# Performance work log

Hardware: AMD Instinct MI355X
Metric: run time of the kernel (lower is better)

The kernel has to match this reference:

```python
import jax, jax.numpy as jnp
import numpy as np

R = 16
ALPHA = 32.0
SCALING = ALPHA / R


def setup_inputs() -> dict:
    key = jax.random.key(0)
    ks = jax.random.split(key, 6)
    B, T, C, O, E = 16, 1500, 1024, 1024, 8
    x = jax.random.normal(ks[0], (B, T, C), dtype=jnp.float32)
    # gate weights per batch element (e.g. softmax-like, but module accepts any)
    w = jax.random.uniform(ks[1], (B, E), dtype=jnp.float32)
    W_base = jax.random.normal(ks[2], (O, C), dtype=jnp.float32) * 0.02
    b_base = jax.random.normal(ks[3], (O,), dtype=jnp.float32) * 0.02
    As = jax.random.normal(ks[4], (E, R, C), dtype=jnp.float32) * 0.02
    Bs = jax.random.normal(ks[5], (E, O, R), dtype=jnp.float32) * 0.02
    return {"x": x, "w": w, "W_base": W_base, "b_base": b_base, "As": As, "Bs": Bs}


def reference(x, w, W_base, b_base, As, Bs):
    # base linear: (B,T,C) @ (C,O) + b
    out = jnp.einsum('btc,oc->bto', x, W_base) + b_base
    # per-expert low-rank: h[b,t,e,r] = x[b,t,:] @ A_e^T
    h = jnp.einsum('btc,erc->bter', x, As)          # (B,T,E,R)
    # y[b,t,e,o] = h @ B_e^T ; gate-weighted sum over experts
    lora = jnp.einsum('bter,eor,be->bto', h, Bs, w)  # (B,T,O)
    return out + lora * SCALING
```

## Files before the change

### kernel.cpp

```cpp
#include <hip/hip_runtime.h>
#include <stdint.h>
#include <stddef.h>


#define B_ 16
#define T_ 1500
#define C_ 1024
#define O_ 1024
#define E_ 8
#define R_ 16
#define ER 128
#define KK 1152
#define BT 24000
#define SCALING 2.0f

typedef __bf16 bf16x8 __attribute__((ext_vector_type(8)));
typedef float f32x4 __attribute__((ext_vector_type(4)));
typedef unsigned short u16;

__device__ inline u16 f2bf(float f) {
  union { float f; unsigned u; } v; v.f = f;
  unsigned u = v.u;
  u += 0x7fff + ((u >> 16) & 1);
  return (u16)(u >> 16);
}

#define GLL(gp, lp)                                                            \
  __builtin_amdgcn_global_load_lds(                                            \
      (const __attribute__((address_space(1))) void*)(gp),                     \
      (__attribute__((address_space(3))) void*)(lp), 16, 0, 0)

__global__ __launch_bounds__(256) void cvt_x(const float4* __restrict__ x,
                                             u16* __restrict__ xp) {
  int i = blockIdx.x * 256 + threadIdx.x;
  float4 v = x[i];
  int row = i >> 8;
  int c = (i & 255) << 2;
  ushort4 o;
  o.x = f2bf(v.x); o.y = f2bf(v.y); o.z = f2bf(v.z); o.w = f2bf(v.w);
  *(ushort4*)(xp + (size_t)row * KK + c) = o;
}

__global__ __launch_bounds__(256) void prep_w(const float* __restrict__ Wb,
                                              const float* __restrict__ Bs,
                                              const float* __restrict__ As,
                                              u16* __restrict__ wp,
                                              u16* __restrict__ ap) {
  int idx = blockIdx.x * 256 + threadIdx.x;
  if (idx < O_ * KK) {
    int o = idx / KK;
    int k = idx - o * KK;
    float v;
    if (k < C_) {
      v = Wb[o * C_ + k];
    } else {
      int j = k - C_;
      v = Bs[((j >> 4) * O_ + o) * R_ + (j & 15)];
    }
    wp[idx] = f2bf(v);
  } else {
    int a = idx - O_ * KK;
    ap[a] = f2bf(As[a]);
  }
}

__global__ __launch_bounds__(256) void h_gemm(u16* __restrict__ xp,
                                              const u16* __restrict__ ab,
                                              const float* __restrict__ w) {
  const int mt = blockIdx.x;
  const int tid = threadIdx.x, lane = tid & 63, wv = tid >> 6;
  const int wrow = wv & 1, wcol = wv >> 1, l15 = lane & 15, quad = lane >> 4;
  const int kx = quad ^ (l15 & 3) ^ ((l15 >> 2) & 3);

  __shared__ u16 lA[128 * 32];
  __shared__ u16 lB[128 * 32];
  const u16* gA = xp + (size_t)mt * 128 * KK;

  f32x4 acc[4][4];
#pragma unroll
  for (int i = 0; i < 4; ++i)
#pragma unroll
    for (int j = 0; j < 4; ++j) acc[i][j] = (f32x4){0.f, 0.f, 0.f, 0.f};

  const int idx0 = tid, idx1 = 256 + tid;
  const int r0 = idx0 >> 2, kc0 = (idx0 & 3) ^ (r0 & 3) ^ ((r0 >> 2) & 3);
  const int r1 = idx1 >> 2, kc1 = (idx1 & 3) ^ (r1 & 3) ^ ((r1 >> 2) & 3);

  for (int kt = 0; kt < C_ / 32; ++kt) {
    const int k0 = kt * 32;
    GLL(gA + (size_t)r0 * KK + k0 + kc0 * 8, &lA[idx0 * 8]);
    GLL(gA + (size_t)r1 * KK + k0 + kc1 * 8, &lA[idx1 * 8]);
    GLL(ab + r0 * C_ + k0 + kc0 * 8, &lB[idx0 * 8]);
    GLL(ab + r1 * C_ + k0 + kc1 * 8, &lB[idx1 * 8]);
    __syncthreads();
    bf16x8 af[4], bfr[4];
#pragma unroll
    for (int i = 0; i < 4; ++i) {
      af[i] = *(const bf16x8*)&lA[(wrow * 64 + i * 16 + l15) * 32 + kx * 8];
      bfr[i] = *(const bf16x8*)&lB[(wcol * 64 + i * 16 + l15) * 32 + kx * 8];
    }
#pragma unroll
    for (int i = 0; i < 4; ++i)
#pragma unroll
      for (int j = 0; j < 4; ++j)
        acc[i][j] = __builtin_amdgcn_mfma_f32_16x16x32_bf16(af[i], bfr[j], acc[i][j], 0, 0, 0);
    __syncthreads();
  }

#pragma unroll
  for (int j = 0; j < 4; ++j) {
    const int col = wcol * 64 + j * 16 + l15;
    const int e = wcol * 4 + j;
#pragma unroll
    for (int i = 0; i < 4; ++i) {
#pragma unroll
      for (int rr = 0; rr < 4; ++rr) {
        const int row = mt * 128 + wrow * 64 + i * 16 + quad * 4 + rr;
        if (row < BT) {
          const int b = row / T_;
          xp[(size_t)row * KK + C_ + col] = f2bf(acc[i][j][rr] * (SCALING * w[b * E_ + e]));
        }
      }
    }
  }
}

__global__ __launch_bounds__(256) void main_gemm(const u16* __restrict__ xp,
                                                 const u16* __restrict__ wp,
                                                 const float* __restrict__ bb,
                                                 float* __restrict__ out) {
  const int id = blockIdx.x;
  const int nt = id & 7;
  const int mt = id >> 3;
  const int tid = threadIdx.x, lane = tid & 63, wv = tid >> 6;
  const int wrow = wv & 1, wcol = wv >> 1, l15 = lane & 15, quad = lane >> 4;
  const int kx = quad ^ (l15 & 3) ^ ((l15 >> 2) & 3);

  __shared__ u16 lA[128 * 32];
  __shared__ u16 lB[128 * 32];
  const u16* gA = xp + (size_t)mt * 128 * KK;
  const u16* gB = wp + (size_t)nt * 128 * KK;

  f32x4 acc[4][4];
#pragma unroll
  for (int i = 0; i < 4; ++i)
#pragma unroll
    for (int j = 0; j < 4; ++j) acc[i][j] = (f32x4){0.f, 0.f, 0.f, 0.f};

  const int idx0 = tid, idx1 = 256 + tid;
  const int r0 = idx0 >> 2, kc0 = (idx0 & 3) ^ (r0 & 3) ^ ((r0 >> 2) & 3);
  const int r1 = idx1 >> 2, kc1 = (idx1 & 3) ^ (r1 & 3) ^ ((r1 >> 2) & 3);

  for (int kt = 0; kt < KK / 32; ++kt) {
    const int k0 = kt * 32;
    GLL(gA + (size_t)r0 * KK + k0 + kc0 * 8, &lA[idx0 * 8]);
    GLL(gA + (size_t)r1 * KK + k0 + kc1 * 8, &lA[idx1 * 8]);
    GLL(gB + (size_t)r0 * KK + k0 + kc0 * 8, &lB[idx0 * 8]);
    GLL(gB + (size_t)r1 * KK + k0 + kc1 * 8, &lB[idx1 * 8]);
    __syncthreads();
    bf16x8 af[4], bfr[4];
#pragma unroll
    for (int i = 0; i < 4; ++i) {
      af[i] = *(const bf16x8*)&lA[(wrow * 64 + i * 16 + l15) * 32 + kx * 8];
      bfr[i] = *(const bf16x8*)&lB[(wcol * 64 + i * 16 + l15) * 32 + kx * 8];
    }
#pragma unroll
    for (int i = 0; i < 4; ++i)
#pragma unroll
      for (int j = 0; j < 4; ++j)
        acc[i][j] = __builtin_amdgcn_mfma_f32_16x16x32_bf16(af[i], bfr[j], acc[i][j], 0, 0, 0);
    __syncthreads();
  }

#pragma unroll
  for (int j = 0; j < 4; ++j) {
    const int col = nt * 128 + wcol * 64 + j * 16 + l15;
    const float bias = bb[col];
#pragma unroll
    for (int i = 0; i < 4; ++i) {
#pragma unroll
      for (int rr = 0; rr < 4; ++rr) {
        const int row = mt * 128 + wrow * 64 + i * 16 + quad * 4 + rr;
        if (row < BT) out[(size_t)row * O_ + col] = acc[i][j][rr] + bias;
      }
    }
  }
}

extern "C" void kernel_launch(void* const* d_in, const int* in_sizes, int n_in,
                              void* d_out, int out_size, void* d_ws, size_t ws_size,
                              hipStream_t stream) {
  const float* x = (const float*)d_in[0];
  const float* w = (const float*)d_in[1];
  const float* Wb = (const float*)d_in[2];
  const float* bb = (const float*)d_in[3];
  const float* As = (const float*)d_in[4];
  const float* Bs = (const float*)d_in[5];
  float* out = (float*)d_out;

  u16* xp = (u16*)d_ws;
  u16* wp = xp + (size_t)BT * KK;
  u16* ap = wp + (size_t)O_ * KK;

  prep_w<<<(O_ * KK + ER * C_) / 256, 256, 0, stream>>>(Wb, Bs, As, wp, ap);
  cvt_x<<<BT * C_ / 1024, 256, 0, stream>>>((const float4*)x, xp);
  h_gemm<<<188, 256, 0, stream>>>(xp, ap, w);
  main_gemm<<<1504, 256, 0, stream>>>(xp, wp, bb, out);
}
```

Baseline: 310.3 us.

## Fuse x bf16 conversion into LoRA h-GEMM and swizzle main GEMM block order

Removes the separate cvt_x kernel. The h-GEMM now reads fp32 x directly, converts it to bf16 in registers, writes it into padded LDS for its own MFMA, and also stores it to xp for the main GEMM. The tile height drops from 128 to 64 rows, so the launch becomes 375 blocks instead of 188. The main GEMM block mapping is regrouped so 8 M-tiles by 8 N-tiles run adjacently for better L2 reuse, with padded blocks exiting early. This saves a full round trip of the bf16 x through global memory and one launch. The cost is non-async loads in the h-GEMM with no load/compute overlap.

Result: faster. 299.3 us (-3.5%).

```diff
diff --git a/kernel.cpp b/kernel.cpp
--- a/kernel.cpp
+++ b/kernel.cpp
@@ -29,17 +29,6 @@
   __builtin_amdgcn_global_load_lds(                                            \
       (const __attribute__((address_space(1))) void*)(gp),                     \
       (__attribute__((address_space(3))) void*)(lp), 16, 0, 0)
-
-__global__ __launch_bounds__(256) void cvt_x(const float4* __restrict__ x,
-                                             u16* __restrict__ xp) {
-  int i = blockIdx.x * 256 + threadIdx.x;
-  float4 v = x[i];
-  int row = i >> 8;
-  int c = (i & 255) << 2;
-  ushort4 o;
-  o.x = f2bf(v.x); o.y = f2bf(v.y); o.z = f2bf(v.z); o.w = f2bf(v.w);
-  *(ushort4*)(xp + (size_t)row * KK + c) = o;
-}
 
 __global__ __launch_bounds__(256) void prep_w(const float* __restrict__ Wb,
                                               const float* __restrict__ Bs,
@@ -64,21 +53,23 @@
   }
 }
 
-__global__ __launch_bounds__(256) void h_gemm(u16* __restrict__ xp,
-                                              const u16* __restrict__ ab,
-                                              const float* __restrict__ w) {
+__global__ __launch_bounds__(256) void cvt_h(const float* __restrict__ x,
+                                             const u16* __restrict__ ab,
+                                             const float* __restrict__ w,
+                                             u16* __restrict__ xp) {
   const int mt = blockIdx.x;
   const int tid = threadIdx.x, lane = tid & 63, wv = tid >> 6;
   const int wrow = wv & 1, wcol = wv >> 1, l15 = lane & 15, quad = lane >> 4;
   const int kx = quad ^ (l15 & 3) ^ ((l15 >> 2) & 3);
 
-  __shared__ u16 lA[128 * 32];
+  __shared__ u16 lA[64 * 40];
   __shared__ u16 lB[128 * 32];
-  const u16* gA = xp + (size_t)mt * 128 * KK;
-
-  f32x4 acc[4][4];
-#pragma unroll
-  for (int i = 0; i < 4; ++i)
+
+  const size_t row0 = (size_t)mt * 64;
+
+  f32x4 acc[2][4];
+#pragma unroll
+  for (int i = 0; i < 2; ++i)
 #pragma unroll
     for (int j = 0; j < 4; ++j) acc[i][j] = (f32x4){0.f, 0.f, 0.f, 0.f};
 
@@ -86,21 +77,33 @@
   const int r0 = idx0 >> 2, kc0 = (idx0 & 3) ^ (r0 & 3) ^ ((r0 >> 2) & 3);
   const int r1 = idx1 >> 2, kc1 = (idx1 & 3) ^ (r1 & 3) ^ ((r1 >> 2) & 3);
 
+  const int xr0 = tid >> 3;
+  const int xr1 = xr0 + 32;
+  const int xc = (tid & 7) * 4;
+
   for (int kt = 0; kt < C_ / 32; ++kt) {
     const int k0 = kt * 32;
-    GLL(gA + (size_t)r0 * KK + k0 + kc0 * 8, &lA[idx0 * 8]);
-    GLL(gA + (size_t)r1 * KK + k0 + kc1 * 8, &lA[idx1 * 8]);
     GLL(ab + r0 * C_ + k0 + kc0 * 8, &lB[idx0 * 8]);
     GLL(ab + r1 * C_ + k0 + kc1 * 8, &lB[idx1 * 8]);
-    __syncthreads();
-    bf16x8 af[4], bfr[4];
-#pragma unroll
-    for (int i = 0; i < 4; ++i) {
-      af[i] = *(const bf16x8*)&lA[(wrow * 64 + i * 16 + l15) * 32 + kx * 8];
-      bfr[i] = *(const bf16x8*)&lB[(wcol * 64 + i * 16 + l15) * 32 + kx * 8];
-    }
-#pragma unroll
-    for (int i = 0; i < 4; ++i)
+    float4 v0 = *(const float4*)&x[(row0 + xr0) * C_ + k0 + xc];
+    float4 v1 = *(const float4*)&x[(row0 + xr1) * C_ + k0 + xc];
+    ushort4 o0, o1;
+    o0.x = f2bf(v0.x); o0.y = f2bf(v0.y); o0.z = f2bf(v0.z); o0.w = f2bf(v0.w);
+    o1.x = f2bf(v1.x); o1.y = f2bf(v1.y); o1.z = f2bf(v1.z); o1.w = f2bf(v1.w);
+    *(ushort4*)&lA[xr0 * 40 + xc] = o0;
+    *(ushort4*)&lA[xr1 * 40 + xc] = o1;
+    *(ushort4*)&xp[(row0 + xr0) * KK + k0 + xc] = o0;
+    *(ushort4*)&xp[(row0 + xr1) * KK + k0 + xc] = o1;
+    __syncthreads();
+    bf16x8 af[2], bfr[4];
+#pragma unroll
+    for (int i = 0; i < 2; ++i)
+      af[i] = *(const bf16x8*)&lA[(wrow * 32 + i * 16 + l15) * 40 + quad * 8];
+#pragma unroll
+    for (int j = 0; j < 4; ++j)
+      bfr[j] = *(const bf16x8*)&lB[(wcol * 64 + j * 16 + l15) * 32 + kx * 8];
+#pragma unroll
+    for (int i = 0; i < 2; ++i)
 #pragma unroll
       for (int j = 0; j < 4; ++j)
         acc[i][j] = __builtin_amdgcn_mfma_f32_16x16x32_bf16(af[i], bfr[j], acc[i][j], 0, 0, 0);
@@ -112,14 +115,12 @@
     const int col = wcol * 64 + j * 16 + l15;
     const int e = wcol * 4 + j;
 #pragma unroll
-    for (int i = 0; i < 4; ++i) {
+    for (int i = 0; i < 2; ++i) {
 #pragma unroll
       for (int rr = 0; rr < 4; ++rr) {
-        const int row = mt * 128 + wrow * 64 + i * 16 + quad * 4 + rr;
-        if (row < BT) {
-          const int b = row / T_;
-          xp[(size_t)row * KK + C_ + col] = f2bf(acc[i][j][rr] * (SCALING * w[b * E_ + e]));
-        }
+        const int row = mt * 64 + wrow * 32 + i * 16 + quad * 4 + rr;
+        const int b = row / T_;
+        xp[(size_t)row * KK + C_ + col] = f2bf(acc[i][j][rr] * (SCALING * w[b * E_ + e]));
       }
     }
   }
@@ -130,8 +131,9 @@
                                                  const float* __restrict__ bb,
                                                  float* __restrict__ out) {
   const int id = blockIdx.x;
-  const int nt = id & 7;
-  const int mt = id >> 3;
+  const int mt = ((id >> 6) << 3) | (id & 7);
+  const int nt = (id >> 3) & 7;
+  if (mt >= 188) return;
   const int tid = threadIdx.x, lane = tid & 63, wv = tid >> 6;
   const int wrow = wv & 1, wcol = wv >> 1, l15 = lane & 15, quad = lane >> 4;
   const int kx = quad ^ (l15 & 3) ^ ((l15 >> 2) & 3);
@@ -203,7 +205,6 @@
   u16* ap = wp + (size_t)O_ * KK;
 
   prep_w<<<(O_ * KK + ER * C_) / 256, 256, 0, stream>>>(Wb, Bs, As, wp, ap);
-  cvt_x<<<BT * C_ / 1024, 256, 0, stream>>>((const float4*)x, xp);
-  h_gemm<<<188, 256, 0, stream>>>(xp, ap, w);
-  main_gemm<<<1504, 256, 0, stream>>>(xp, wp, bb, out);
-}
+  cvt_h<<<375, 256, 0, stream>>>(x, ap, w, xp);
+  main_gemm<<<1536, 256, 0, stream>>>(xp, wp, bb, out);
+}
```
